# Optimization experiments

Hardware: AMD Instinct MI355X
Metric: run time of the kernel (lower is better)

Reference implementation:

```python
import jax, jax.numpy as jnp
import numpy as np

NUM_OBJ_CLS = 151


def setup_inputs() -> dict:
    key = jax.random.key(0)
    ks = jax.random.split(key, 12)
    N, H, E, U, P, R = 6144, 512, 49152, 2048, 4096, 51
    return {
        "edge_ctx": jax.random.normal(ks[0], (N, H), jnp.float32),
        "union_features": jax.random.normal(ks[1], (E, U), jnp.float32),
        "W_post_emb": jax.random.normal(ks[2], (H, 2 * H), jnp.float32) * (H ** -0.5),
        "b_post_emb": jnp.zeros((2 * H,), jnp.float32),
        "W_post_cat": jax.random.normal(ks[3], (2 * H, P), jnp.float32) * ((2 * H) ** -0.5),
        "b_post_cat": jnp.zeros((P,), jnp.float32),
        "W_up": jax.random.normal(ks[4], (U, P), jnp.float32) * (U ** -0.5),
        "b_up": jnp.zeros((P,), jnp.float32),
        "W_rel": jax.random.normal(ks[5], (P, R), jnp.float32) * (P ** -0.5),
        "b_rel": jnp.zeros((R,), jnp.float32),
        "freq_table": jax.random.normal(ks[6], (NUM_OBJ_CLS * NUM_OBJ_CLS, R), jnp.float32),
        "obj_preds": jax.random.randint(ks[7], (N,), 0, NUM_OBJ_CLS, jnp.int64),
        "pair_idx": jax.random.randint(ks[8], (E, 2), 0, N, jnp.int64),
    }


def reference(edge_ctx, union_features, W_post_emb, b_post_emb, W_post_cat,
              b_post_cat, W_up, b_up, W_rel, b_rel, freq_table,
              obj_preds, pair_idx):
    N, H = edge_ctx.shape
    # post_emb -> split into head/tail representations [N, H] each
    edge_rep = (edge_ctx @ W_post_emb + b_post_emb).reshape(N, 2, H)
    head_rep, tail_rep = edge_rep[:, 0], edge_rep[:, 1]
    # gather per-pair head/tail reps and concat -> [E, 2H]
    prod_rep = jnp.concatenate(
        (head_rep[pair_idx[:, 0]], tail_rep[pair_idx[:, 1]]), axis=-1)
    prod_rep = prod_rep @ W_post_cat + b_post_cat            # [E, P]
    # union feature up-projection (union_single_not_match) and gating multiply
    prod_rep = prod_rep * (union_features @ W_up + b_up)     # [E, P]
    rel_dists = prod_rep @ W_rel + b_rel                     # [E, R]
    # frequency-bias lookup indexed by (head_class, tail_class)
    bias_idx = obj_preds[pair_idx[:, 0]] * NUM_OBJ_CLS + obj_preds[pair_idx[:, 1]]
    rel_dists = rel_dists + freq_table[bias_idx]
    return rel_dists
```

## Files before the change

kernel.cpp:

```cpp
#include <hip/hip_runtime.h>

typedef unsigned short u16;
typedef __attribute__((ext_vector_type(4))) float f32x4;
typedef __attribute__((ext_vector_type(4))) u16 u16x4;
typedef __attribute__((ext_vector_type(8))) u16 u16x8;
typedef __attribute__((ext_vector_type(8))) short short8;

__device__ __forceinline__ u16 f2bf(float f) {
  unsigned int u = __builtin_bit_cast(unsigned int, f);
  u += 0x7FFFu + ((u >> 16) & 1u);
  return (u16)(u >> 16);
}
__device__ __forceinline__ float bf2f(u16 b) {
  unsigned int u = ((unsigned int)b) << 16;
  return __builtin_bit_cast(float, u);
}

__device__ __forceinline__ void gld16(const void* g, void* l) {
  __builtin_amdgcn_global_load_lds(
      (const __attribute__((address_space(1))) unsigned int*)g,
      (__attribute__((address_space(3))) unsigned int*)l, 16, 0, 0);
}

template <int N>
__device__ __forceinline__ void boundary() {
  asm volatile("s_waitcnt vmcnt(%0)" ::"n"(N) : "memory");
  __builtin_amdgcn_s_barrier();
  asm volatile("" ::: "memory");
  __builtin_amdgcn_sched_barrier(0);
}


__global__ __launch_bounds__(256) void cvt_f32_bf16(const float* __restrict__ s,
                                                    u16* __restrict__ d, long n4) {
  long stride = (long)gridDim.x * 256;
  for (long i = (long)blockIdx.x * 256 + threadIdx.x; i < n4; i += stride) {
    f32x4 v = *(const f32x4*)(s + i * 4);
    u16x4 o = {f2bf(v.x), f2bf(v.y), f2bf(v.z), f2bf(v.w)};
    *(u16x4*)(d + i * 4) = o;
  }
}

__global__ __launch_bounds__(256) void transpose_f32_bf16(const float* __restrict__ src,
                                                          u16* __restrict__ dst,
                                                          int R, int C, int CP) {
  __shared__ float tile[32][33];
  int r0 = blockIdx.x * 32, c0 = blockIdx.y * 32;
  int tx = threadIdx.x & 31, ty = threadIdx.x >> 5;
#pragma unroll
  for (int i = 0; i < 32; i += 8) {
    int r = r0 + ty + i, c = c0 + tx;
    tile[ty + i][tx] = (r < R && c < C) ? src[(size_t)r * C + c] : 0.f;
  }
  __syncthreads();
#pragma unroll
  for (int i = 0; i < 32; i += 8) {
    int c = c0 + ty + i, r = r0 + tx;
    if (c < CP && r < R) dst[(size_t)c * R + r] = f2bf(tile[tx][ty + i]);
  }
}


template <int NROW>
__device__ __forceinline__ void stage_direct(const u16* __restrict__ src, int ld,
                                             int kcol0, u16* lds, int tid) {
#pragma unroll
  for (int it = 0; it < NROW / 32; ++it) {
    int idx = it * 256 + tid;
    int row = idx >> 3, c = idx & 7;
    int cc = c ^ (row & 7);
    gld16(src + (size_t)row * ld + kcol0 + cc * 8, (char*)lds + idx * 16);
  }
}

template <int MI>
__device__ __forceinline__ void mma_step(const char* As, const char* Bs, int arow0,
                                         int brow0, int lane, f32x4 acc[MI][4]) {
  int r = lane & 15, q = lane >> 4;
#pragma unroll
  for (int ks = 0; ks < 2; ++ks) {
    short8 a[MI], b[4];
#pragma unroll
    for (int i = 0; i < MI; ++i) {
      int row = arow0 + i * 16 + r;
      a[i] = *(const short8*)(As + row * 128 + ((((ks << 2) + q) ^ (row & 7)) << 4));
    }
#pragma unroll
    for (int j = 0; j < 4; ++j) {
      int row = brow0 + j * 16 + r;
      b[j] = *(const short8*)(Bs + row * 128 + ((((ks << 2) + q) ^ (row & 7)) << 4));
    }
#pragma unroll
    for (int i = 0; i < MI; ++i)
#pragma unroll
      for (int j = 0; j < 4; ++j)
        acc[i][j] = __builtin_amdgcn_mfma_f32_16x16x32_bf16(a[i], b[j], acc[i][j], 0, 0, 0);
  }
}


__global__ __launch_bounds__(256) void gemm1(const u16* __restrict__ ec,
                                             const u16* __restrict__ WpeT,
                                             const float* __restrict__ bpe,
                                             u16* __restrict__ head,
                                             u16* __restrict__ tail) {
  __shared__ __align__(16) u16 As[128 * 64];
  __shared__ __align__(16) u16 Bs[128 * 64];
  int tid = threadIdx.x, lane = tid & 63, wave = tid >> 6;
  int wrow = wave >> 1, wcol = wave & 1;
  int m0 = blockIdx.x * 128, n0 = blockIdx.y * 128;
  f32x4 z = {0.f, 0.f, 0.f, 0.f};
  f32x4 acc[4][4];
#pragma unroll
  for (int i = 0; i < 4; ++i)
#pragma unroll
    for (int j = 0; j < 4; ++j) acc[i][j] = z;

  for (int kb = 0; kb < 8; ++kb) {
    stage_direct<128>(ec + (size_t)m0 * 512, 512, kb * 64, As, tid);
    stage_direct<128>(WpeT + (size_t)n0 * 512, 512, kb * 64, Bs, tid);
    __syncthreads();
    mma_step<4>((const char*)As, (const char*)Bs, wrow * 64, wcol * 64, lane, acc);
    __syncthreads();
  }
  int r = lane & 15, q = lane >> 4;
#pragma unroll
  for (int i = 0; i < 4; ++i) {
    int e = m0 + wrow * 64 + i * 16 + q * 4;
#pragma unroll
    for (int j = 0; j < 4; ++j) {
      int c = n0 + wcol * 64 + j * 16 + r;
      float bb = bpe[c];
#pragma unroll
      for (int g = 0; g < 4; ++g) {
        float v = acc[i][j][g] + bb;
        if (c < 512) head[(size_t)(e + g) * 512 + c] = f2bf(v);
        else         tail[(size_t)(e + g) * 512 + (c - 512)] = f2bf(v);
      }
    }
  }
}


__global__ __launch_bounds__(256) void gemm_hp(const u16* __restrict__ A,
                                               const u16* __restrict__ BT,
                                               u16* __restrict__ P) {
  __shared__ __align__(16) u16 As[128 * 64];
  __shared__ __align__(16) u16 Bs[128 * 64];
  int tid = threadIdx.x, lane = tid & 63, wave = tid >> 6;
  int wrow = wave >> 1, wcol = wave & 1;
  int m0 = blockIdx.x * 128, n0 = blockIdx.y * 128;
  f32x4 z = {0.f, 0.f, 0.f, 0.f};
  f32x4 acc[4][4];
#pragma unroll
  for (int i = 0; i < 4; ++i)
#pragma unroll
    for (int j = 0; j < 4; ++j) acc[i][j] = z;

  for (int kb = 0; kb < 8; ++kb) {
    stage_direct<128>(A + (size_t)m0 * 512, 512, kb * 64, As, tid);
    stage_direct<128>(BT + (size_t)n0 * 512, 512, kb * 64, Bs, tid);
    __syncthreads();
    mma_step<4>((const char*)As, (const char*)Bs, wrow * 64, wcol * 64, lane, acc);
    __syncthreads();
  }
  int r = lane & 15, q = lane >> 4;
#pragma unroll
  for (int i = 0; i < 4; ++i) {
    int e = m0 + wrow * 64 + i * 16 + q * 4;
#pragma unroll
    for (int j = 0; j < 4; ++j) {
      int c = n0 + wcol * 64 + j * 16 + r;
#pragma unroll
      for (int g = 0; g < 4; ++g)
        P[(size_t)(e + g) * 4096 + c] = f2bf(acc[i][j][g]);
    }
  }
}


__global__ __launch_bounds__(512, 2) void gemm_union_fuse4(
    const u16* __restrict__ U, const u16* __restrict__ WupT,
    const float* __restrict__ bup, const float* __restrict__ bpc,
    const u16* __restrict__ Hp, const u16* __restrict__ Tp,
    const int* __restrict__ pair, const u16* __restrict__ WrelT,
    u16* __restrict__ Pp) {
  extern __shared__ __align__(16) u16 lds[];
  const int tid = threadIdx.x, lane = tid & 63, wave = tid >> 6;
  const int wm = wave >> 2, wn = wave & 3;
  const int r = lane & 15, q = lane >> 4;

  int bid = blockIdx.x;
  int xcd = bid & 7, seq = bid >> 3;
  int st = seq >> 5, within = seq & 31;
  int gst = xcd * 12 + st;
  int nsuper = gst / 24, msuper = gst % 24;
  int m0 = (msuper * 8 + (within >> 2)) * 256;
  int n0 = (nsuper * 4 + (within & 3)) * 256;

  const u16* Apanel = U + (size_t)m0 * 2048;
  const u16* Bpanel = WupT + (size_t)n0 * 2048;

  f32x4 acc[8][4];
  f32x4 z = {0.f, 0.f, 0.f, 0.f};
#pragma unroll
  for (int i = 0; i < 8; ++i)
#pragma unroll
    for (int j = 0; j < 4; ++j) acc[i][j] = z;

  auto STAGE = [&](int buf, int mat, int kt, int kh) {
    const u16* src = mat ? Bpanel : Apanel;
#pragma unroll
    for (int it = 0; it < 2; ++it) {
      int id = it * 512 + tid;
      int row = id >> 2, c4 = id & 3;
      gld16(src + (size_t)row * 2048 + kt * 64 + kh * 32 + ((c4 ^ ((row >> 1) & 3)) << 3),
            lds + ((((buf << 1) | mat) << 1 | kh) << 13) + id * 8);
    }
  };
  auto LDA = [&](int buf, int kh, int mi) -> short8 {
    int row = wm * 128 + mi * 16 + r;
    return *(const short8*)(lds + (((buf << 1) << 1 | kh) << 13) + row * 32 +
                            ((q ^ ((r >> 1) & 3)) << 3));
  };
  auto LDB = [&](int buf, int kh, int nj) -> short8 {
    int row = wn * 64 + nj * 16 + r;
    return *(const short8*)(lds + ((((buf << 1) | 1) << 1 | kh) << 13) + row * 32 +
                            ((q ^ ((r >> 1) & 3)) << 3));
  };

  STAGE(0, 0, 0, 0);
  STAGE(0, 1, 0, 0);
  STAGE(0, 0, 0, 1);
  STAGE(0, 1, 0, 1);
  boundary<4>();

  short8 a[4], b[4];
  const int NT = 32;
  for (int t = 0; t < NT; ++t) {
    int cur = t & 1, nxt = cur ^ 1;
    bool more = (t < NT - 1);

#pragma unroll
    for (int nj = 0; nj < 4; ++nj) b[nj] = LDB(cur, 0, nj);
#pragma unroll
    for (int mi = 0; mi < 4; ++mi) a[mi] = LDA(cur, 0, mi);
    if (more) STAGE(nxt, 0, t + 1, 0);
    __builtin_amdgcn_s_setprio(1);
#pragma unroll
    for (int mi = 0; mi < 4; ++mi)
#pragma unroll
      for (int nj = 0; nj < 4; ++nj)
        acc[mi][nj] = __builtin_amdgcn_mfma_f32_16x16x32_bf16(a[mi], b[nj], acc[mi][nj], 0, 0, 0);
    __builtin_amdgcn_s_setprio(0);

#pragma unroll
    for (int mi = 0; mi < 4; ++mi) a[mi] = LDA(cur, 0, mi + 4);
    if (more) STAGE(nxt, 1, t + 1, 0);
    __builtin_amdgcn_s_setprio(1);
#pragma unroll
    for (int mi = 0; mi < 4; ++mi)
#pragma unroll
      for (int nj = 0; nj < 4; ++nj)
        acc[mi + 4][nj] = __builtin_amdgcn_mfma_f32_16x16x32_bf16(a[mi], b[nj], acc[mi + 4][nj], 0, 0, 0);
    __builtin_amdgcn_s_setprio(0);

    if (t == NT - 1) boundary<0>(); else boundary<4>();

#pragma unroll
    for (int nj = 0; nj < 4; ++nj) b[nj] = LDB(cur, 1, nj);
#pragma unroll
    for (int mi = 0; mi < 4; ++mi) a[mi] = LDA(cur, 1, mi);
    if (more) STAGE(nxt, 0, t + 1, 1);
    __builtin_amdgcn_s_setprio(1);
#pragma unroll
    for (int mi = 0; mi < 4; ++mi)
#pragma unroll
      for (int nj = 0; nj < 4; ++nj)
        acc[mi][nj] = __builtin_amdgcn_mfma_f32_16x16x32_bf16(a[mi], b[nj], acc[mi][nj], 0, 0, 0);
    __builtin_amdgcn_s_setprio(0);

#pragma unroll
    for (int mi = 0; mi < 4; ++mi) a[mi] = LDA(cur, 1, mi + 4);
    if (more) STAGE(nxt, 1, t + 1, 1);
    __builtin_amdgcn_s_setprio(1);
#pragma unroll
    for (int mi = 0; mi < 4; ++mi)
#pragma unroll
      for (int nj = 0; nj < 4; ++nj)
        acc[mi + 4][nj] = __builtin_amdgcn_mfma_f32_16x16x32_bf16(a[mi], b[nj], acc[mi + 4][nj], 0, 0, 0);
    __builtin_amdgcn_s_setprio(0);

    if (more) boundary<4>();
  }

  __syncthreads();

  u16* Uw = lds + (wave << 13);
#pragma unroll
  for (int mi = 0; mi < 8; ++mi) {
#pragma unroll
    for (int nj = 0; nj < 4; ++nj) {
      int col = nj * 16 + r;
      float bb = bup[n0 + wn * 64 + col];
#pragma unroll
      for (int g = 0; g < 4; ++g) {
        int rw = mi * 16 + q * 4 + g;
        int byte_off = rw * 128 + ((((col >> 3) ^ (rw & 7)) << 4)) + (col & 7) * 2;
        *(u16*)((char*)Uw + byte_off) = f2bf(acc[mi][nj][g] + bb);
      }
    }
  }
  asm volatile("s_waitcnt lgkmcnt(0)" ::: "memory");
  __builtin_amdgcn_sched_barrier(0);

  int c0 = n0 + wn * 64;
#pragma unroll
  for (int rr = 0; rr < 2; ++rr) {
    int lr = lane * 2 + rr;
    int e = m0 + wm * 128 + lr;
    int h = pair[2 * e], tt = pair[2 * e + 1];
    const u16* hp = Hp + (size_t)h * 4096 + c0;
    const u16* tp = Tp + (size_t)tt * 4096 + c0;
#pragma unroll
    for (int ch = 0; ch < 8; ++ch) {
      u16x8 hv = *(const u16x8*)(hp + ch * 8);
      u16x8 tv = *(const u16x8*)(tp + ch * 8);
      u16* slot = (u16*)((char*)Uw + lr * 128 + ((ch ^ (lr & 7)) << 4));
      u16x8 uv = *(u16x8*)slot;
      u16x8 o;
#pragma unroll
      for (int k = 0; k < 8; ++k) {
        float p = bf2f(hv[k]) + bf2f(tv[k]) + bpc[c0 + ch * 8 + k];
        o[k] = f2bf(bf2f(uv[k]) * p);
      }
      *(u16x8*)slot = o;
    }
  }
  __syncthreads();

  f32x4 acc2[2][4];
#pragma unroll
  for (int i = 0; i < 2; ++i)
#pragma unroll
    for (int j = 0; j < 4; ++j) acc2[i][j] = z;

#pragma unroll
  for (int ks = 0; ks < 8; ++ks) {
    int wn_k = ks >> 1;
    int cb = (ks & 1) * 4;
    short8 a2[2], b2[4];
#pragma unroll
    for (int i = 0; i < 2; ++i) {
      int rr2 = wave * 32 + i * 16 + r;
      int reg = ((rr2 >> 7) << 2) | wn_k;
      int lr2 = rr2 & 127;
      int ch = cb + q;
      a2[i] = *(const short8*)((char*)lds + reg * 16384 + lr2 * 128 +
                               ((ch ^ (lr2 & 7)) << 4));
    }
#pragma unroll
    for (int j = 0; j < 4; ++j)
      b2[j] = *(const short8*)(WrelT + (size_t)(j * 16 + r) * 4096 + n0 + ks * 32 + q * 8);
#pragma unroll
    for (int i = 0; i < 2; ++i)
#pragma unroll
      for (int j = 0; j < 4; ++j)
        acc2[i][j] = __builtin_amdgcn_mfma_f32_16x16x32_bf16(a2[i], b2[j], acc2[i][j], 0, 0, 0);
  }

  int nt = n0 >> 8;
#pragma unroll
  for (int i = 0; i < 2; ++i) {
#pragma unroll
    for (int j = 0; j < 4; ++j) {
      int col = j * 16 + r;
#pragma unroll
      for (int g = 0; g < 4; ++g) {
        int e = m0 + wave * 32 + i * 16 + q * 4 + g;
        Pp[((size_t)nt * 49152 + e) * 64 + col] = f2bf(acc2[i][j][g]);
      }
    }
  }
}


__global__ __launch_bounds__(256) void reduce_out(const u16* __restrict__ Pp,
                                                  const float* __restrict__ brel,
                                                  const float* __restrict__ freq,
                                                  const int* __restrict__ obj,
                                                  const int* __restrict__ pair,
                                                  float* __restrict__ out) {
  int e = blockIdx.x * 4 + (threadIdx.x >> 6);
  int c = threadIdx.x & 63;
  const u16* p = Pp + (size_t)e * 64 + c;
  float s = 0.f;
#pragma unroll
  for (int nt = 0; nt < 16; ++nt) s += bf2f(p[(size_t)nt * 49152 * 64]);
  if (c < 51) {
    int bidx = obj[pair[2 * e]] * 151 + obj[pair[2 * e + 1]];
    out[(size_t)e * 51 + c] = s + brel[c] + freq[(size_t)bidx * 51 + c];
  }
}


extern "C" void kernel_launch(void* const* d_in, const int* in_sizes, int n_in,
                              void* d_out, int out_size, void* d_ws, size_t ws_size,
                              hipStream_t stream) {
  const float* edge_ctx = (const float*)d_in[0];
  const float* unionf   = (const float*)d_in[1];
  const float* Wpe      = (const float*)d_in[2];
  const float* bpe      = (const float*)d_in[3];
  const float* Wpc      = (const float*)d_in[4];
  const float* bpc      = (const float*)d_in[5];
  const float* Wup      = (const float*)d_in[6];
  const float* bup      = (const float*)d_in[7];
  const float* Wrel     = (const float*)d_in[8];
  const float* brel     = (const float*)d_in[9];
  const float* freq     = (const float*)d_in[10];
  const int*   obj      = (const int*)d_in[11];
  const int*   pair     = (const int*)d_in[12];
  float* out = (float*)d_out;

  u16* ws = (u16*)d_ws;
  u16* Pp      = ws;
  u16* ub      = ws + 201326592;
  u16* ec      = ws + 301989888;
  u16* head    = ws + 305135616;
  u16* tail    = ws + 308281344;
  u16* WpeT    = ws + 311427072;
  u16* WpcTopT = ws + 311951360;
  u16* WpcBotT = ws + 314048512;
  u16* WupT    = ws + 316145664;
  u16* WrelT   = ws + 324534272;
  u16* Hp      = ws + 324796416;
  u16* Tp      = ws + 349962240;

  cvt_f32_bf16<<<768, 256, 0, stream>>>(edge_ctx, ec, 786432);
  cvt_f32_bf16<<<4096, 256, 0, stream>>>(unionf, ub, 25165824);
  transpose_f32_bf16<<<dim3(16, 32), 256, 0, stream>>>(Wpe, WpeT, 512, 1024, 1024);
  transpose_f32_bf16<<<dim3(16, 128), 256, 0, stream>>>(Wpc, WpcTopT, 512, 4096, 4096);
  transpose_f32_bf16<<<dim3(16, 128), 256, 0, stream>>>(Wpc + (size_t)512 * 4096, WpcBotT, 512, 4096, 4096);
  transpose_f32_bf16<<<dim3(64, 128), 256, 0, stream>>>(Wup, WupT, 2048, 4096, 4096);
  transpose_f32_bf16<<<dim3(128, 2), 256, 0, stream>>>(Wrel, WrelT, 4096, 51, 64);

  gemm1<<<dim3(48, 8), 256, 0, stream>>>(ec, WpeT, bpe, head, tail);
  gemm_hp<<<dim3(48, 32), 256, 0, stream>>>(head, WpcTopT, Hp);
  gemm_hp<<<dim3(48, 32), 256, 0, stream>>>(tail, WpcBotT, Tp);
  gemm_union_fuse4<<<3072, 512, 131072, stream>>>(ub, WupT, bup, bpc, Hp, Tp, pair, WrelT, Pp);
  reduce_out<<<12288, 256, 0, stream>>>(Pp, brel, freq, obj, pair, out);
}
```

Baseline: 1.241 ms.

## Deepen GEMM pipeline with three in-flight half-tile stages and register double-buffering

Restructures the main K loop of the union up-projection GEMM so global-to-LDS loads run three half-tiles ahead instead of one full tile. A and B fragments are double-buffered in registers, with each MFMA group delayed by one phase so LDS reads overlap the previous phase's matrix math. sched_barrier calls pin the interleave. The intent is to hide global load latency and LDS read latency behind MFMA work, at the cost of more VGPRs and more complex wait counting around the buffer reuse.

```diff
diff --git a/kernel.cpp b/kernel.cpp
--- a/kernel.cpp
+++ b/kernel.cpp
@@ -218,6 +218,10 @@
             lds + ((((buf << 1) | mat) << 1 | kh) << 13) + id * 8);
     }
   };
+  auto GROUP = [&](int kt, int kh) {
+    STAGE(kt & 1, 0, kt, kh);
+    STAGE(kt & 1, 1, kt, kh);
+  };
   auto LDA = [&](int buf, int kh, int mi) -> short8 {
     int row = wm * 128 + mi * 16 + r;
     return *(const short8*)(lds + (((buf << 1) << 1 | kh) << 13) + row * 32 +
@@ -229,70 +233,69 @@
                             ((q ^ ((r >> 1) & 3)) << 3));
   };
 
-  STAGE(0, 0, 0, 0);
-  STAGE(0, 1, 0, 0);
-  STAGE(0, 0, 0, 1);
-  STAGE(0, 1, 0, 1);
-  boundary<4>();
-
-  short8 a[4], b[4];
+  short8 A0[4], A1[4], B0[4], B1[4];
+
+  auto MMA_LO = [&](short8* A, short8* B) {
+    __builtin_amdgcn_s_setprio(1);
+#pragma unroll
+    for (int mi = 0; mi < 4; ++mi)
+#pragma unroll
+      for (int nj = 0; nj < 4; ++nj)
+        acc[mi][nj] = __builtin_amdgcn_mfma_f32_16x16x32_bf16(A[mi], B[nj], acc[mi][nj], 0, 0, 0);
+    __builtin_amdgcn_s_setprio(0);
+  };
+  auto MMA_HI = [&](short8* A, short8* B) {
+    __builtin_amdgcn_s_setprio(1);
+#pragma unroll
+    for (int mi = 0; mi < 4; ++mi)
+#pragma unroll
+      for (int nj = 0; nj < 4; ++nj)
+        acc[mi + 4][nj] = __builtin_amdgcn_mfma_f32_16x16x32_bf16(A[mi], B[nj], acc[mi + 4][nj], 0, 0, 0);
+    __builtin_amdgcn_s_setprio(0);
+  };
+
   const int NT = 32;
+
+  GROUP(0, 0);
+  GROUP(0, 1);
+  GROUP(1, 0);
+  boundary<8>();
+
   for (int t = 0; t < NT; ++t) {
-    int cur = t & 1, nxt = cur ^ 1;
-    bool more = (t < NT - 1);
-
-#pragma unroll
-    for (int nj = 0; nj < 4; ++nj) b[nj] = LDB(cur, 0, nj);
-#pragma unroll
-    for (int mi = 0; mi < 4; ++mi) a[mi] = LDA(cur, 0, mi);
-    if (more) STAGE(nxt, 0, t + 1, 0);
-    __builtin_amdgcn_s_setprio(1);
-#pragma unroll
-    for (int mi = 0; mi < 4; ++mi)
-#pragma unroll
-      for (int nj = 0; nj < 4; ++nj)
-        acc[mi][nj] = __builtin_amdgcn_mfma_f32_16x16x32_bf16(a[mi], b[nj], acc[mi][nj], 0, 0, 0);
-    __builtin_amdgcn_s_setprio(0);
-
-#pragma unroll
-    for (int mi = 0; mi < 4; ++mi) a[mi] = LDA(cur, 0, mi + 4);
-    if (more) STAGE(nxt, 1, t + 1, 0);
-    __builtin_amdgcn_s_setprio(1);
-#pragma unroll
-    for (int mi = 0; mi < 4; ++mi)
-#pragma unroll
-      for (int nj = 0; nj < 4; ++nj)
-        acc[mi + 4][nj] = __builtin_amdgcn_mfma_f32_16x16x32_bf16(a[mi], b[nj], acc[mi + 4][nj], 0, 0, 0);
-    __builtin_amdgcn_s_setprio(0);
-
-    if (t == NT - 1) boundary<0>(); else boundary<4>();
-
-#pragma unroll
-    for (int nj = 0; nj < 4; ++nj) b[nj] = LDB(cur, 1, nj);
-#pragma unroll
-    for (int mi = 0; mi < 4; ++mi) a[mi] = LDA(cur, 1, mi);
-    if (more) STAGE(nxt, 0, t + 1, 1);
-    __builtin_amdgcn_s_setprio(1);
-#pragma unroll
-    for (int mi = 0; mi < 4; ++mi)
-#pragma unroll
-      for (int nj = 0; nj < 4; ++nj)
-        acc[mi][nj] = __builtin_amdgcn_mfma_f32_16x16x32_bf16(a[mi], b[nj], acc[mi][nj], 0, 0, 0);
-    __builtin_amdgcn_s_setprio(0);
-
-#pragma unroll
-    for (int mi = 0; mi < 4; ++mi) a[mi] = LDA(cur, 1, mi + 4);
-    if (more) STAGE(nxt, 1, t + 1, 1);
-    __builtin_amdgcn_s_setprio(1);
-#pragma unroll
-    for (int mi = 0; mi < 4; ++mi)
-#pragma unroll
-      for (int nj = 0; nj < 4; ++nj)
-        acc[mi + 4][nj] = __builtin_amdgcn_mfma_f32_16x16x32_bf16(a[mi], b[nj], acc[mi + 4][nj], 0, 0, 0);
-    __builtin_amdgcn_s_setprio(0);
-
-    if (more) boundary<4>();
-  }
+    int cur = t & 1;
+
+#pragma unroll
+    for (int nj = 0; nj < 4; ++nj) B0[nj] = LDB(cur, 0, nj);
+#pragma unroll
+    for (int mi = 0; mi < 4; ++mi) A0[mi] = LDA(cur, 0, mi);
+    __builtin_amdgcn_sched_barrier(0);
+    if (t > 0) MMA_HI(A1, B1);
+
+#pragma unroll
+    for (int mi = 0; mi < 4; ++mi) A1[mi] = LDA(cur, 0, mi + 4);
+    if (t + 1 < NT) GROUP(t + 1, 1);
+    __builtin_amdgcn_sched_barrier(0);
+    MMA_LO(A0, B0);
+
+    if (t == NT - 1) boundary<0>(); else boundary<8>();
+
+#pragma unroll
+    for (int nj = 0; nj < 4; ++nj) B1[nj] = LDB(cur, 1, nj);
+#pragma unroll
+    for (int mi = 0; mi < 4; ++mi) A0[mi] = LDA(cur, 1, mi);
+    __builtin_amdgcn_sched_barrier(0);
+    MMA_HI(A1, B0);
+
+#pragma unroll
+    for (int mi = 0; mi < 4; ++mi) A1[mi] = LDA(cur, 1, mi + 4);
+    if (t + 2 < NT) GROUP(t + 2, 0);
+    __builtin_amdgcn_sched_barrier(0);
+    MMA_LO(A0, B1);
+
+    if (t + 2 < NT) boundary<8>();
+    else if (t + 1 < NT) boundary<4>();
+  }
+  MMA_HI(A1, B1);
 
   __syncthreads();
 
```

New measurement: 1.257 ms. No clear change (+1.3%).

## Halve fused union GEMM N-tile and K-step to double occupancy

Applied to the files above, without the earlier changes.

Shrinks the fused union GEMM tile from 256x256 to 256x128 and the K step from 64 to 32. This halves LDS per block to 64KB and the accumulator registers, so launch bounds can request 4 blocks per CU, and the grid doubles to 6144 blocks. The intent is more latency hiding through occupancy. In exchange, A-panel reuse drops: each union row panel is reloaded twice as often. There are twice as many K iterations, each with a full barrier, and twice as many partial rel_dist slices for reduce_out to write and sum.

```diff
diff --git a/kernel.cpp b/kernel.cpp
--- a/kernel.cpp
+++ b/kernel.cpp
@@ -179,7 +179,7 @@
 }
 
 
-__global__ __launch_bounds__(512, 2) void gemm_union_fuse4(
+__global__ __launch_bounds__(512, 4) void gemm_union_fuse4(
     const u16* __restrict__ U, const u16* __restrict__ WupT,
     const float* __restrict__ bup, const float* __restrict__ bpc,
     const u16* __restrict__ Hp, const u16* __restrict__ Tp,
@@ -193,120 +193,92 @@
   int bid = blockIdx.x;
   int xcd = bid & 7, seq = bid >> 3;
   int st = seq >> 5, within = seq & 31;
-  int gst = xcd * 12 + st;
+  int gst = xcd * 24 + st;
   int nsuper = gst / 24, msuper = gst % 24;
   int m0 = (msuper * 8 + (within >> 2)) * 256;
-  int n0 = (nsuper * 4 + (within & 3)) * 256;
+  int n0 = (nsuper * 4 + (within & 3)) * 128;
 
   const u16* Apanel = U + (size_t)m0 * 2048;
   const u16* Bpanel = WupT + (size_t)n0 * 2048;
 
-  f32x4 acc[8][4];
+  f32x4 acc[8][2];
   f32x4 z = {0.f, 0.f, 0.f, 0.f};
 #pragma unroll
   for (int i = 0; i < 8; ++i)
 #pragma unroll
-    for (int j = 0; j < 4; ++j) acc[i][j] = z;
-
-  auto STAGE = [&](int buf, int mat, int kt, int kh) {
-    const u16* src = mat ? Bpanel : Apanel;
+    for (int j = 0; j < 2; ++j) acc[i][j] = z;
+
+  auto STAGEA = [&](int buf, int kt) {
 #pragma unroll
     for (int it = 0; it < 2; ++it) {
       int id = it * 512 + tid;
       int row = id >> 2, c4 = id & 3;
-      gld16(src + (size_t)row * 2048 + kt * 64 + kh * 32 + ((c4 ^ ((row >> 1) & 3)) << 3),
-            lds + ((((buf << 1) | mat) << 1 | kh) << 13) + id * 8);
+      gld16(Apanel + (size_t)row * 2048 + kt * 32 + ((c4 ^ ((row >> 1) & 3)) << 3),
+            lds + buf * 8192 + id * 8);
     }
   };
-  auto LDA = [&](int buf, int kh, int mi) -> short8 {
+  auto STAGEB = [&](int buf, int kt) {
+    int row = tid >> 2, c4 = tid & 3;
+    gld16(Bpanel + (size_t)row * 2048 + kt * 32 + ((c4 ^ ((row >> 1) & 3)) << 3),
+          lds + 16384 + buf * 4096 + tid * 8);
+  };
+  auto LDA = [&](int buf, int mi) -> short8 {
     int row = wm * 128 + mi * 16 + r;
-    return *(const short8*)(lds + (((buf << 1) << 1 | kh) << 13) + row * 32 +
+    return *(const short8*)(lds + buf * 8192 + row * 32 + ((q ^ ((r >> 1) & 3)) << 3));
+  };
+  auto LDB = [&](int buf, int nj) -> short8 {
+    int row = wn * 32 + nj * 16 + r;
+    return *(const short8*)(lds + 16384 + buf * 4096 + row * 32 +
                             ((q ^ ((r >> 1) & 3)) << 3));
   };
-  auto LDB = [&](int buf, int kh, int nj) -> short8 {
-    int row = wn * 64 + nj * 16 + r;
-    return *(const short8*)(lds + ((((buf << 1) | 1) << 1 | kh) << 13) + row * 32 +
-                            ((q ^ ((r >> 1) & 3)) << 3));
-  };
-
-  STAGE(0, 0, 0, 0);
-  STAGE(0, 1, 0, 0);
-  STAGE(0, 0, 0, 1);
-  STAGE(0, 1, 0, 1);
-  boundary<4>();
-
-  short8 a[4], b[4];
-  const int NT = 32;
+
+  STAGEA(0, 0); STAGEB(0, 0);
+  boundary<0>();
+
+  const int NT = 64;
   for (int t = 0; t < NT; ++t) {
     int cur = t & 1, nxt = cur ^ 1;
     bool more = (t < NT - 1);
-
-#pragma unroll
-    for (int nj = 0; nj < 4; ++nj) b[nj] = LDB(cur, 0, nj);
-#pragma unroll
-    for (int mi = 0; mi < 4; ++mi) a[mi] = LDA(cur, 0, mi);
-    if (more) STAGE(nxt, 0, t + 1, 0);
+    if (more) { STAGEA(nxt, t + 1); STAGEB(nxt, t + 1); }
+
+    short8 a[4], b[2];
+#pragma unroll
+    for (int nj = 0; nj < 2; ++nj) b[nj] = LDB(cur, nj);
+#pragma unroll
+    for (int mi = 0; mi < 4; ++mi) a[mi] = LDA(cur, mi);
     __builtin_amdgcn_s_setprio(1);
 #pragma unroll
     for (int mi = 0; mi < 4; ++mi)
 #pragma unroll
-      for (int nj = 0; nj < 4; ++nj)
+      for (int nj = 0; nj < 2; ++nj)
         acc[mi][nj] = __builtin_amdgcn_mfma_f32_16x16x32_bf16(a[mi], b[nj], acc[mi][nj], 0, 0, 0);
     __builtin_amdgcn_s_setprio(0);
-
-#pragma unroll
-    for (int mi = 0; mi < 4; ++mi) a[mi] = LDA(cur, 0, mi + 4);
-    if (more) STAGE(nxt, 1, t + 1, 0);
+#pragma unroll
+    for (int mi = 0; mi < 4; ++mi) a[mi] = LDA(cur, mi + 4);
     __builtin_amdgcn_s_setprio(1);
 #pragma unroll
     for (int mi = 0; mi < 4; ++mi)
 #pragma unroll
-      for (int nj = 0; nj < 4; ++nj)
+      for (int nj = 0; nj < 2; ++nj)
         acc[mi + 4][nj] = __builtin_amdgcn_mfma_f32_16x16x32_bf16(a[mi], b[nj], acc[mi + 4][nj], 0, 0, 0);
     __builtin_amdgcn_s_setprio(0);
 
-    if (t == NT - 1) boundary<0>(); else boundary<4>();
-
-#pragma unroll
-    for (int nj = 0; nj < 4; ++nj) b[nj] = LDB(cur, 1, nj);
-#pragma unroll
-    for (int mi = 0; mi < 4; ++mi) a[mi] = LDA(cur, 1, mi);
-    if (more) STAGE(nxt, 0, t + 1, 1);
-    __builtin_amdgcn_s_setprio(1);
-#pragma unroll
-    for (int mi = 0; mi < 4; ++mi)
-#pragma unroll
-      for (int nj = 0; nj < 4; ++nj)
-        acc[mi][nj] = __builtin_amdgcn_mfma_f32_16x16x32_bf16(a[mi], b[nj], acc[mi][nj], 0, 0, 0);
-    __builtin_amdgcn_s_setprio(0);
-
-#pragma unroll
-    for (int mi = 0; mi < 4; ++mi) a[mi] = LDA(cur, 1, mi + 4);
-    if (more) STAGE(nxt, 1, t + 1, 1);
-    __builtin_amdgcn_s_setprio(1);
-#pragma unroll
-    for (int mi = 0; mi < 4; ++mi)
-#pragma unroll
-      for (int nj = 0; nj < 4; ++nj)
-        acc[mi + 4][nj] = __builtin_amdgcn_mfma_f32_16x16x32_bf16(a[mi], b[nj], acc[mi + 4][nj], 0, 0, 0);
-    __builtin_amdgcn_s_setprio(0);
-
-    if (more) boundary<4>();
+    if (more) boundary<0>();
   }
 
   __syncthreads();
 
-  u16* Uw = lds + (wave << 13);
+  u16* Uw = lds + ((wm * 4 + wn) << 12);
 #pragma unroll
   for (int mi = 0; mi < 8; ++mi) {
 #pragma unroll
-    for (int nj = 0; nj < 4; ++nj) {
+    for (int nj = 0; nj < 2; ++nj) {
       int col = nj * 16 + r;
-      float bb = bup[n0 + wn * 64 + col];
+      float bb = bup[n0 + wn * 32 + col];
 #pragma unroll
       for (int g = 0; g < 4; ++g) {
         int rw = mi * 16 + q * 4 + g;
-        int byte_off = rw * 128 + ((((col >> 3) ^ (rw & 7)) << 4)) + (col & 7) * 2;
+        int byte_off = rw * 64 + ((((col >> 3) ^ ((rw >> 1) & 3)) << 4)) + (col & 7) * 2;
         *(u16*)((char*)Uw + byte_off) = f2bf(acc[mi][nj][g] + bb);
       }
     }
@@ -314,7 +286,7 @@
   asm volatile("s_waitcnt lgkmcnt(0)" ::: "memory");
   __builtin_amdgcn_sched_barrier(0);
 
-  int c0 = n0 + wn * 64;
+  int c0 = n0 + wn * 32;
 #pragma unroll
   for (int rr = 0; rr < 2; ++rr) {
     int lr = lane * 2 + rr;
@@ -323,10 +295,10 @@
     const u16* hp = Hp + (size_t)h * 4096 + c0;
     const u16* tp = Tp + (size_t)tt * 4096 + c0;
 #pragma unroll
-    for (int ch = 0; ch < 8; ++ch) {
+    for (int ch = 0; ch < 4; ++ch) {
       u16x8 hv = *(const u16x8*)(hp + ch * 8);
       u16x8 tv = *(const u16x8*)(tp + ch * 8);
-      u16* slot = (u16*)((char*)Uw + lr * 128 + ((ch ^ (lr & 7)) << 4));
+      u16* slot = (u16*)((char*)Uw + lr * 64 + ((ch ^ ((lr >> 1) & 3)) << 4));
       u16x8 uv = *(u16x8*)slot;
       u16x8 o;
 #pragma unroll
@@ -346,18 +318,15 @@
     for (int j = 0; j < 4; ++j) acc2[i][j] = z;
 
 #pragma unroll
-  for (int ks = 0; ks < 8; ++ks) {
-    int wn_k = ks >> 1;
-    int cb = (ks & 1) * 4;
+  for (int ks = 0; ks < 4; ++ks) {
     short8 a2[2], b2[4];
 #pragma unroll
     for (int i = 0; i < 2; ++i) {
       int rr2 = wave * 32 + i * 16 + r;
-      int reg = ((rr2 >> 7) << 2) | wn_k;
+      int reg = ((rr2 >> 7) << 2) | ks;
       int lr2 = rr2 & 127;
-      int ch = cb + q;
-      a2[i] = *(const short8*)((char*)lds + reg * 16384 + lr2 * 128 +
-                               ((ch ^ (lr2 & 7)) << 4));
+      a2[i] = *(const short8*)((char*)lds + reg * 8192 + lr2 * 64 +
+                               ((q ^ ((lr2 >> 1) & 3)) << 4));
     }
 #pragma unroll
     for (int j = 0; j < 4; ++j)
@@ -369,7 +338,7 @@
         acc2[i][j] = __builtin_amdgcn_mfma_f32_16x16x32_bf16(a2[i], b2[j], acc2[i][j], 0, 0, 0);
   }
 
-  int nt = n0 >> 8;
+  int nt = n0 >> 7;
 #pragma unroll
   for (int i = 0; i < 2; ++i) {
 #pragma unroll
@@ -396,7 +365,7 @@
   const u16* p = Pp + (size_t)e * 64 + c;
   float s = 0.f;
 #pragma unroll
-  for (int nt = 0; nt < 16; ++nt) s += bf2f(p[(size_t)nt * 49152 * 64]);
+  for (int nt = 0; nt < 32; ++nt) s += bf2f(p[(size_t)nt * 49152 * 64]);
   if (c < 51) {
     int bidx = obj[pair[2 * e]] * 151 + obj[pair[2 * e + 1]];
     out[(size_t)e * 51 + c] = s + brel[c] + freq[(size_t)bidx * 51 + c];
@@ -447,6 +416,6 @@
   gemm1<<<dim3(48, 8), 256, 0, stream>>>(ec, WpeT, bpe, head, tail);
   gemm_hp<<<dim3(48, 32), 256, 0, stream>>>(head, WpcTopT, Hp);
   gemm_hp<<<dim3(48, 32), 256, 0, stream>>>(tail, WpcBotT, Tp);
-  gemm_union_fuse4<<<3072, 512, 131072, stream>>>(ub, WupT, bup, bpc, Hp, Tp, pair, WrelT, Pp);
+  gemm_union_fuse4<<<6144, 512, 65536, stream>>>(ub, WupT, bup, bpc, Hp, Tp, pair, WrelT, Pp);
   reduce_out<<<12288, 256, 0, stream>>>(Pp, brel, freq, obj, pair, out);
 }
```

Result: slower. 1.321 ms (+6.5%).

## Load W_up B-fragments directly from global into registers, stage only A via LDS

Applied to the files above, without the earlier changes.

The union-projection GEMM kernel no longer stages the W_up^T tile through LDS. Each wave loads its B fragments straight from global memory into registers, double-buffered as b0/b1 and prefetched one k-step ahead. Only the A panel still goes through LDS with global_load_lds. The loop is unrolled by two with compile-time buffer indices, which turns LDS address arithmetic into constants. This halves LDS staging traffic and ds_reads, at the cost of more global/L2 reads of B across waves, extra VGPRs, and changed vmcnt waits.

```diff
diff --git a/kernel.cpp b/kernel.cpp
--- a/kernel.cpp
+++ b/kernel.cpp
@@ -5,6 +5,8 @@
 typedef __attribute__((ext_vector_type(4))) u16 u16x4;
 typedef __attribute__((ext_vector_type(8))) u16 u16x8;
 typedef __attribute__((ext_vector_type(8))) short short8;
+
+template <int V> struct IC { static constexpr int value = V; };
 
 __device__ __forceinline__ u16 f2bf(float f) {
   unsigned int u = __builtin_bit_cast(unsigned int, f);
@@ -198,9 +200,6 @@
   int m0 = (msuper * 8 + (within >> 2)) * 256;
   int n0 = (nsuper * 4 + (within & 3)) * 256;
 
-  const u16* Apanel = U + (size_t)m0 * 2048;
-  const u16* Bpanel = WupT + (size_t)n0 * 2048;
-
   f32x4 acc[8][4];
   f32x4 z = {0.f, 0.f, 0.f, 0.f};
 #pragma unroll
@@ -208,90 +207,96 @@
 #pragma unroll
     for (int j = 0; j < 4; ++j) acc[i][j] = z;
 
-  auto STAGE = [&](int buf, int mat, int kt, int kh) {
-    const u16* src = mat ? Bpanel : Apanel;
-#pragma unroll
-    for (int it = 0; it < 2; ++it) {
-      int id = it * 512 + tid;
-      int row = id >> 2, c4 = id & 3;
-      gld16(src + (size_t)row * 2048 + kt * 64 + kh * 32 + ((c4 ^ ((row >> 1) & 3)) << 3),
-            lds + ((((buf << 1) | mat) << 1 | kh) << 13) + id * 8);
-    }
+  int chunk = (q ^ ((r >> 1) & 3)) << 4;
+  const char* cA0 = (const char*)lds + (wm * 128 + r) * 64 + chunk;
+  const char* cA1 = cA0 + 32768;
+
+  int srow = tid >> 2, sc4 = tid & 3;
+  int sswz = (sc4 ^ ((srow >> 1) & 3)) * 8;
+  const u16* gA0 = U + (size_t)(m0 + srow) * 2048 + sswz;
+  const u16* gA1 = U + (size_t)(m0 + 128 + srow) * 2048 + sswz;
+  const u16* gB = WupT + (size_t)(n0 + wn * 64 + r) * 2048 + q * 8;
+
+  auto STGA = [&](int khu , int qb ) {
+    gld16(gA0 + khu, lds + qb + tid * 8);
+    gld16(gA1 + khu, lds + qb + 4096 + tid * 8);
   };
-  auto LDA = [&](int buf, int kh, int mi) -> short8 {
-    int row = wm * 128 + mi * 16 + r;
-    return *(const short8*)(lds + (((buf << 1) << 1 | kh) << 13) + row * 32 +
-                            ((q ^ ((r >> 1) & 3)) << 3));
+
+  short8 a[4], b0[4], b1[4];
+
+#pragma unroll
+  for (int nj = 0; nj < 4; ++nj) b0[nj] = *(const short8*)(gB + (size_t)nj * 32768);
+#pragma unroll
+  for (int nj = 0; nj < 4; ++nj) b1[nj] = *(const short8*)(gB + 32 + (size_t)nj * 32768);
+  STGA(0, 0);
+  STGA(32, 8192);
+  gA0 += 64; gA1 += 64;
+  boundary<2>();
+
+  auto kstep = [&](auto curc, bool more) {
+    constexpr int CUR = decltype(curc)::value;
+    constexpr int NXT = CUR ^ 1;
+    const char* pa = CUR ? cA1 : cA0;
+
+#pragma unroll
+    for (int mi = 0; mi < 4; ++mi) a[mi] = *(const short8*)(pa + mi * 1024);
+    if (more) STGA(0, (NXT * 2 + 0) * 8192);
+    __builtin_amdgcn_s_setprio(1);
+#pragma unroll
+    for (int mi = 0; mi < 4; ++mi)
+#pragma unroll
+      for (int nj = 0; nj < 4; ++nj)
+        acc[mi][nj] = __builtin_amdgcn_mfma_f32_16x16x32_bf16(a[mi], b0[nj], acc[mi][nj], 0, 0, 0);
+    __builtin_amdgcn_s_setprio(0);
+
+#pragma unroll
+    for (int mi = 0; mi < 4; ++mi) a[mi] = *(const short8*)(pa + (mi + 4) * 1024);
+    __builtin_amdgcn_s_setprio(1);
+#pragma unroll
+    for (int mi = 0; mi < 4; ++mi)
+#pragma unroll
+      for (int nj = 0; nj < 4; ++nj)
+        acc[mi + 4][nj] = __builtin_amdgcn_mfma_f32_16x16x32_bf16(a[mi], b0[nj], acc[mi + 4][nj], 0, 0, 0);
+    __builtin_amdgcn_s_setprio(0);
+    if (more) {
+#pragma unroll
+      for (int nj = 0; nj < 4; ++nj) b0[nj] = *(const short8*)(gB + 64 + (size_t)nj * 32768);
+    }
+
+    if (more) boundary<6>(); else boundary<0>();
+
+#pragma unroll
+    for (int mi = 0; mi < 4; ++mi) a[mi] = *(const short8*)(pa + 16384 + mi * 1024);
+    if (more) STGA(32, (NXT * 2 + 1) * 8192);
+    __builtin_amdgcn_s_setprio(1);
+#pragma unroll
+    for (int mi = 0; mi < 4; ++mi)
+#pragma unroll
+      for (int nj = 0; nj < 4; ++nj)
+        acc[mi][nj] = __builtin_amdgcn_mfma_f32_16x16x32_bf16(a[mi], b1[nj], acc[mi][nj], 0, 0, 0);
+    __builtin_amdgcn_s_setprio(0);
+
+#pragma unroll
+    for (int mi = 0; mi < 4; ++mi) a[mi] = *(const short8*)(pa + 16384 + (mi + 4) * 1024);
+    __builtin_amdgcn_s_setprio(1);
+#pragma unroll
+    for (int mi = 0; mi < 4; ++mi)
+#pragma unroll
+      for (int nj = 0; nj < 4; ++nj)
+        acc[mi + 4][nj] = __builtin_amdgcn_mfma_f32_16x16x32_bf16(a[mi], b1[nj], acc[mi + 4][nj], 0, 0, 0);
+    __builtin_amdgcn_s_setprio(0);
+    if (more) {
+#pragma unroll
+      for (int nj = 0; nj < 4; ++nj) b1[nj] = *(const short8*)(gB + 96 + (size_t)nj * 32768);
+    }
+
+    gA0 += 64; gA1 += 64; gB += 64;
+    if (more) boundary<6>();
   };
-  auto LDB = [&](int buf, int kh, int nj) -> short8 {
-    int row = wn * 64 + nj * 16 + r;
-    return *(const short8*)(lds + ((((buf << 1) | 1) << 1 | kh) << 13) + row * 32 +
-                            ((q ^ ((r >> 1) & 3)) << 3));
-  };
-
-  STAGE(0, 0, 0, 0);
-  STAGE(0, 1, 0, 0);
-  STAGE(0, 0, 0, 1);
-  STAGE(0, 1, 0, 1);
-  boundary<4>();
-
-  short8 a[4], b[4];
-  const int NT = 32;
-  for (int t = 0; t < NT; ++t) {
-    int cur = t & 1, nxt = cur ^ 1;
-    bool more = (t < NT - 1);
-
-#pragma unroll
-    for (int nj = 0; nj < 4; ++nj) b[nj] = LDB(cur, 0, nj);
-#pragma unroll
-    for (int mi = 0; mi < 4; ++mi) a[mi] = LDA(cur, 0, mi);
-    if (more) STAGE(nxt, 0, t + 1, 0);
-    __builtin_amdgcn_s_setprio(1);
-#pragma unroll
-    for (int mi = 0; mi < 4; ++mi)
-#pragma unroll
-      for (int nj = 0; nj < 4; ++nj)
-        acc[mi][nj] = __builtin_amdgcn_mfma_f32_16x16x32_bf16(a[mi], b[nj], acc[mi][nj], 0, 0, 0);
-    __builtin_amdgcn_s_setprio(0);
-
-#pragma unroll
-    for (int mi = 0; mi < 4; ++mi) a[mi] = LDA(cur, 0, mi + 4);
-    if (more) STAGE(nxt, 1, t + 1, 0);
-    __builtin_amdgcn_s_setprio(1);
-#pragma unroll
-    for (int mi = 0; mi < 4; ++mi)
-#pragma unroll
-      for (int nj = 0; nj < 4; ++nj)
-        acc[mi + 4][nj] = __builtin_amdgcn_mfma_f32_16x16x32_bf16(a[mi], b[nj], acc[mi + 4][nj], 0, 0, 0);
-    __builtin_amdgcn_s_setprio(0);
-
-    if (t == NT - 1) boundary<0>(); else boundary<4>();
-
-#pragma unroll
-    for (int nj = 0; nj < 4; ++nj) b[nj] = LDB(cur, 1, nj);
-#pragma unroll
-    for (int mi = 0; mi < 4; ++mi) a[mi] = LDA(cur, 1, mi);
-    if (more) STAGE(nxt, 0, t + 1, 1);
-    __builtin_amdgcn_s_setprio(1);
-#pragma unroll
-    for (int mi = 0; mi < 4; ++mi)
-#pragma unroll
-      for (int nj = 0; nj < 4; ++nj)
-        acc[mi][nj] = __builtin_amdgcn_mfma_f32_16x16x32_bf16(a[mi], b[nj], acc[mi][nj], 0, 0, 0);
-    __builtin_amdgcn_s_setprio(0);
-
-#pragma unroll
-    for (int mi = 0; mi < 4; ++mi) a[mi] = LDA(cur, 1, mi + 4);
-    if (more) STAGE(nxt, 1, t + 1, 1);
-    __builtin_amdgcn_s_setprio(1);
-#pragma unroll
-    for (int mi = 0; mi < 4; ++mi)
-#pragma unroll
-      for (int nj = 0; nj < 4; ++nj)
-        acc[mi + 4][nj] = __builtin_amdgcn_mfma_f32_16x16x32_bf16(a[mi], b[nj], acc[mi + 4][nj], 0, 0, 0);
-    __builtin_amdgcn_s_setprio(0);
-
-    if (more) boundary<4>();
+
+  for (int tt = 0; tt < 16; ++tt) {
+    kstep(IC<0>{}, true);
+    kstep(IC<1>{}, tt < 15);
   }
 
   __syncthreads();
```

Result: slower. 1.615 ms (+30.2%).
